# Kernel optimization log

Measured on AMD Instinct MI355X. Metric: run time of the kernel, lower is better.

The kernel has to match this reference:

```python
import jax, jax.numpy as jnp
import numpy as np

D_MODEL = 1024
NUM_HEADS = 16
THETA = 10000.0
NEG = -1000000.0  # masked_fill value used by the torch code


def _rope(x, token_positions, theta):
    # x: [B, H, S, d_head]; token_positions: [S] int
    d_k = x.shape[-1]
    half = d_k // 2
    j = jnp.arange(half, dtype=jnp.float32)
    inv_freq = theta ** (-(2.0 * j) / d_k)                      # [half]
    ang = token_positions.astype(jnp.float32)[:, None] * inv_freq  # [S, half]
    cos = jnp.cos(ang)
    sin = jnp.sin(ang)
    xp = x.reshape(x.shape[:-1] + (half, 2))  # adjacent pairs (pc, 2)
    x0, x1 = xp[..., 0], xp[..., 1]
    o0 = x0 * cos - x1 * sin
    o1 = x0 * sin + x1 * cos
    out = jnp.stack([o0, o1], axis=-1)
    return out.reshape(x.shape)


def setup_inputs() -> dict:
    key = jax.random.key(0)
    k0, k1, k2 = jax.random.split(key, 3)
    B, S, D = 2, 2048, D_MODEL
    std = (2.0 / (D + D)) ** 0.5
    X = jax.random.normal(k0, (B, S, D), dtype=jnp.float32)
    QKV_weights = jax.random.normal(k1, (3 * D, D), dtype=jnp.float32) * std
    O_weights = jax.random.normal(k2, (D, D), dtype=jnp.float32) * std
    token_positions = jnp.arange(S, dtype=jnp.int32)
    return {"X": X, "token_positions": token_positions,
            "QKV_weights": QKV_weights, "O_weights": O_weights}


def reference(X, token_positions, QKV_weights, O_weights):
    B, S, D = X.shape
    H = NUM_HEADS
    dh = D // H
    qkv = jnp.einsum('od,bsd->bso', QKV_weights, X)  # [B, S, 3D]
    Q, K, V = jnp.split(qkv, 3, axis=-1)

    def split_heads(t):
        return t.reshape(B, S, H, dh).transpose(0, 2, 1, 3)  # [B,H,S,dh]

    Q, K, V = split_heads(Q), split_heads(K), split_heads(V)
    Q = _rope(Q, token_positions, THETA)
    K = _rope(K, token_positions, THETA)

    scores = (jnp.einsum('bhqd,bhkd->bhqk', Q, K) / jnp.sqrt(jnp.float32(dh))).astype(jnp.float32)
    causal = jnp.tril(jnp.ones((S, S), dtype=bool))
    scores = jnp.where(causal, scores, NEG)
    probs = jax.nn.softmax(scores, axis=-1)
    attn = jnp.einsum('bhqk,bhkd->bhqd', probs, V.astype(jnp.float32)).astype(Q.dtype)
    attn = attn.transpose(0, 2, 1, 3).reshape(B, S, D)
    return jnp.einsum('od,bsd->bso', O_weights, attn)
```

## Files before the change

### kernel.cpp

```cpp
#include <hip/hip_runtime.h>
#include <math.h>

#define S_LEN 2048

using bf16x8  = __attribute__((ext_vector_type(8))) short;
using shortx4 = __attribute__((ext_vector_type(4))) short;
using f32x4   = __attribute__((ext_vector_type(4))) float;
using uintx4  = __attribute__((ext_vector_type(4))) unsigned;
using uintx2  = __attribute__((ext_vector_type(2))) unsigned;

static __device__ __forceinline__ short f2bf(float f) {
  unsigned u = __float_as_uint(f);
  u += 0x7fffu + ((u >> 16) & 1u);
  return (short)(u >> 16);
}

#if __has_builtin(__builtin_amdgcn_cvt_pk_bf16_f32)
using bf16x2_t = __attribute__((ext_vector_type(2))) __bf16;
static __device__ __forceinline__ unsigned pkbf(float a, float b) {
  bf16x2_t v = __builtin_amdgcn_cvt_pk_bf16_f32(a, b);
  return __builtin_bit_cast(unsigned, v);
}
#else
static __device__ __forceinline__ unsigned pkbf(float a, float b) {
  return (unsigned)(unsigned short)f2bf(a) | ((unsigned)(unsigned short)f2bf(b) << 16);
}
#endif

#define GLD_LDS16(gptr, lptr)                                                  \
  __builtin_amdgcn_global_load_lds(                                            \
      (__attribute__((address_space(1))) void*)(gptr),                         \
      (__attribute__((address_space(3))) void*)(lptr), 16, 0, 0)

#define EXP2_SHIFT 20.0f

static __device__ __forceinline__ f32x4 exp2s4(f32x4 a) {
  return (f32x4){__builtin_amdgcn_exp2f(a[0] - EXP2_SHIFT),
                 __builtin_amdgcn_exp2f(a[1] - EXP2_SHIFT),
                 __builtin_amdgcn_exp2f(a[2] - EXP2_SHIFT),
                 __builtin_amdgcn_exp2f(a[3] - EXP2_SHIFT)};
}

static __device__ __forceinline__ int sigma64(int k) {
  return (k & 0x20) | ((k & 0x0C) << 1) | ((k & 0x10) >> 2) | (k & 3);
}

__global__ __launch_bounds__(256) void init_kernel(const float* __restrict__ X,
                                                   const float* __restrict__ W1,
                                                   const float* __restrict__ W2,
                                                   const int* __restrict__ tok,
                                                   short* __restrict__ Xb,
                                                   short* __restrict__ W1b,
                                                   short* __restrict__ W2b,
                                                   float2* __restrict__ table) {
  if (blockIdx.x < 4096) {
    size_t idx = (size_t)(blockIdx.x * 256 + threadIdx.x) * 8;
    const float* src;
    short* dst;
    size_t off;
    if (idx < 4194304) { src = X; dst = Xb; off = idx; }
    else if (idx < 4194304 + 3145728) { src = W1; dst = W1b; off = idx - 4194304; }
    else { src = W2; dst = W2b; off = idx - (4194304 + 3145728); }
    float4 a = *(const float4*)(src + off);
    float4 b = *(const float4*)(src + off + 4);
    bf16x8 o = {f2bf(a.x), f2bf(a.y), f2bf(a.z), f2bf(a.w),
                f2bf(b.x), f2bf(b.y), f2bf(b.z), f2bf(b.w)};
    *(bf16x8*)(dst + off) = o;
  } else {
    int i = (blockIdx.x - 4096) * 256 + threadIdx.x;
    int s = i >> 5, j = i & 31;
    double pos = (double)tok[s];
    double ang = pos * pow(10000.0, -(double)j / 32.0);
    table[i] = make_float2((float)cos(ang), (float)sin(ang));
  }
}

template <int BM, typename OutT, int EPI>
__global__ __launch_bounds__(256) void gemm_ll(const short* __restrict__ A,
                                               const short* __restrict__ B,
                                               OutT* __restrict__ C,
                                               const float2* __restrict__ tab,
                                               short* __restrict__ Qb,
                                               short* __restrict__ Kb,
                                               short* __restrict__ VT,
                                               int M, int N, int K) {
  constexpr int MI = BM / 32;
  constexpr int AI = BM / 64;
  __shared__ short As[BM * 32];
  __shared__ short Bs[128 * 32];
  const int tid  = threadIdx.x;
  const int lane = tid & 63;
  const int wv   = tid >> 6;
  const int wm   = (wv >> 1) * (BM / 2);
  const int wn   = (wv & 1) * 64;
  const int m16  = lane & 15;
  const int q4   = lane >> 4;

  const int nwg = gridDim.x * gridDim.y;
  int bid = blockIdx.y * gridDim.x + blockIdx.x;
  bid = (bid & 7) * (nwg >> 3) + (bid >> 3);
  const int rowBase = (bid / gridDim.x) * BM;
  const int colBase = (bid % gridDim.x) * 128;

  const int lrow = lane >> 2;
  const int lchk = (lane & 3) ^ ((lane >> 3) & 3);
  const int fsw  = (q4 ^ ((m16 >> 1) & 3)) * 8;

  f32x4 acc[MI][4];
#pragma unroll
  for (int i = 0; i < MI; ++i)
#pragma unroll
    for (int j = 0; j < 4; ++j) acc[i][j] = (f32x4){0.f, 0.f, 0.f, 0.f};

  const short* Agl = A + (size_t)rowBase * K;
  const short* Bgl = B + (size_t)colBase * K;

  for (int kk = 0; kk < K; kk += 32) {
#pragma unroll
    for (int i = 0; i < AI; ++i) {
      const int r0 = (wv * AI + i) * 16;
      GLD_LDS16(Agl + (size_t)(r0 + lrow) * K + kk + lchk * 8, &As[r0 * 32]);
    }
#pragma unroll
    for (int i = 0; i < 2; ++i) {
      const int r0 = (wv * 2 + i) * 16;
      GLD_LDS16(Bgl + (size_t)(r0 + lrow) * K + kk + lchk * 8, &Bs[r0 * 32]);
    }
    __syncthreads();

    bf16x8 af[MI], bfv[4];
#pragma unroll
    for (int mi = 0; mi < MI; ++mi)
      af[mi] = *(const bf16x8*)&As[(wm + mi * 16 + m16) * 32 + fsw];
#pragma unroll
    for (int ni = 0; ni < 4; ++ni)
      bfv[ni] = *(const bf16x8*)&Bs[(wn + ni * 16 + m16) * 32 + fsw];
#pragma unroll
    for (int mi = 0; mi < MI; ++mi)
#pragma unroll
      for (int ni = 0; ni < 4; ++ni)
        acc[mi][ni] = __builtin_amdgcn_mfma_f32_16x16x32_bf16(af[mi], bfv[ni], acc[mi][ni], 0, 0, 0);
    __syncthreads();
  }

  if constexpr (EPI == 0) {
#pragma unroll
    for (int mi = 0; mi < MI; ++mi)
#pragma unroll
      for (int ni = 0; ni < 4; ++ni) {
        const int rbase = rowBase + wm + mi * 16 + q4 * 4;
        const int cidx  = colBase + wn + ni * 16 + m16;
#pragma unroll
        for (int r = 0; r < 4; ++r) {
          float v = acc[mi][ni][r];
          if constexpr (sizeof(OutT) == 2)
            C[(size_t)(rbase + r) * N + cidx] = (OutT)f2bf(v);
          else
            C[(size_t)(rbase + r) * N + cidx] = (OutT)v;
        }
      }
  } else {
    const int sect = colBase >> 10;
#pragma unroll
    for (int mi = 0; mi < MI; ++mi)
#pragma unroll
      for (int ni = 0; ni < 4; ++ni) {
        const int col = colBase + wn + ni * 16 + m16;
        const int rb  = rowBase + wm + mi * 16 + q4 * 4;
        if (sect == 2) {
          const int hd = col - 2048;
          const int h = hd >> 6, d = hd & 63;
          const int b = rb >> 11, s0 = rb & (S_LEN - 1);
          shortx4 pk4 = {f2bf(acc[mi][ni][0]), f2bf(acc[mi][ni][1]),
                         f2bf(acc[mi][ni][2]), f2bf(acc[mi][ni][3])};
          *(shortx4*)(VT + ((size_t)((b * 16 + h) * 64 + d)) * S_LEN +
                      (s0 & ~63) + sigma64(s0 & 63)) = pk4;
        } else {
          const int cc = col & 1023;
          const int h = cc >> 6, d = cc & 63, j = d >> 1;
          const float sgn = (m16 & 1) ? 1.f : -1.f;
          short* dstp = (sect == 0) ? Qb : Kb;
          const float scl = (sect == 0) ? (0.125f * 1.44269504f) : 1.f;
#pragma unroll
          for (int r = 0; r < 4; ++r) {
            const int row = rb + r;
            const int s = row & (S_LEN - 1), bidx = row >> 11;
            float2 cs = tab[s * 32 + j];
            float self = acc[mi][ni][r];
            float part = __shfl_xor(self, 1);
            float o = (self * cs.x + sgn * part * cs.y) * scl;
            dstp[((size_t)((bidx * 16 + h) * S_LEN + s)) * 64 + d] = f2bf(o);
          }
        }
      }
  }
}

__global__ __launch_bounds__(256, 2) void attn_mfma(const short* __restrict__ Qb,
                                                    const short* __restrict__ Kb,
                                                    const short* __restrict__ VT,
                                                    short* __restrict__ attnb) {
  __shared__ __align__(16) short Smem[9216];
  short* Ks = Smem;
  short* Vs = Smem + 64 * 72;
  const int tid  = threadIdx.x;
  const int lane = tid & 63;
  const int w    = tid >> 6;
  const int m16  = lane & 15;
  const int q4   = lane >> 4;
  const int bh   = blockIdx.x;
  const int jtx  = blockIdx.y;
  const int jt   = (jtx < 8) ? (15 - jtx) : (jtx - 8);
  const int b    = bh >> 4, h = bh & 15;
  const short* Qh = Qb + (size_t)bh * S_LEN * 64;
  const short* Kh = Kb + (size_t)bh * S_LEN * 64;
  const short* Vh = VT + (size_t)bh * 64 * S_LEN;

  const int srow = tid >> 3;
  const int seg  = tid & 7;

  const bf16x8 ones = {16256, 16256, 16256, 16256, 16256, 16256, 16256, 16256};

  const int q0 = jt * 128;
  const int ktiles = 2 * jt + 2;

  bf16x8 qf[2][2];
#pragma unroll
  for (int n = 0; n < 2; ++n)
#pragma unroll
    for (int ks = 0; ks < 2; ++ks)
      qf[n][ks] = *(const bf16x8*)(Qh + (size_t)(q0 + w * 32 + n * 16 + m16) * 64 + ks * 32 + q4 * 8);

  f32x4 O[2][4], Lacc[2];
#pragma unroll
  for (int n = 0; n < 2; ++n) {
    Lacc[n] = (f32x4){0.f, 0.f, 0.f, 0.f};
#pragma unroll
    for (int c = 0; c < 4; ++c) O[n][c] = (f32x4){0.f, 0.f, 0.f, 0.f};
  }

  bf16x8 kst[2], vst[2];
#pragma unroll
  for (int i = 0; i < 2; ++i) {
    kst[i] = *(const bf16x8*)(Kh + (size_t)(i * 32 + srow) * 64 + seg * 8);
    vst[i] = *(const bf16x8*)(Vh + (size_t)(i * 32 + srow) * S_LEN + seg * 8);
  }

  for (int t = 0; t < ktiles; ++t) {
#pragma unroll
    for (int i = 0; i < 2; ++i) {
      *(bf16x8*)&Ks[(i * 32 + srow) * 72 + seg * 8] = kst[i];
      *(bf16x8*)&Vs[(i * 32 + srow) * 72 + seg * 8] = vst[i];
    }
    __syncthreads();

    if (t + 1 < ktiles) {
#pragma unroll
      for (int i = 0; i < 2; ++i) {
        kst[i] = *(const bf16x8*)(Kh + (size_t)((t + 1) * 64 + i * 32 + srow) * 64 + seg * 8);
        vst[i] = *(const bf16x8*)(Vh + (size_t)(i * 32 + srow) * S_LEN + (t + 1) * 64 + seg * 8);
      }
    }

    f32x4 sc[2][4];
#pragma unroll
    for (int n = 0; n < 2; ++n)
#pragma unroll
      for (int c = 0; c < 4; ++c) sc[n][c] = (f32x4){0.f, 0.f, 0.f, 0.f};
    __builtin_amdgcn_s_setprio(1);
#pragma unroll
    for (int ks = 0; ks < 2; ++ks) {
#pragma unroll
      for (int c = 0; c < 4; ++c) {
        bf16x8 kf = *(const bf16x8*)&Ks[(c * 16 + m16) * 72 + ks * 32 + q4 * 8];
#pragma unroll
        for (int n = 0; n < 2; ++n)
          sc[n][c] = __builtin_amdgcn_mfma_f32_16x16x32_bf16(kf, qf[n][ks], sc[n][c], 0, 0, 0);
      }
    }
    __builtin_amdgcn_s_setprio(0);

    if (t >= ktiles - 2) {
#pragma unroll
      for (int n = 0; n < 2; ++n)
#pragma unroll
        for (int c = 0; c < 4; ++c) {
          const int qg = q0 + w * 32 + n * 16 + m16;
#pragma unroll
          for (int rr = 0; rr < 4; ++rr) {
            const int kg = t * 64 + c * 16 + q4 * 4 + rr;
            if (kg > qg) sc[n][c][rr] = -1e30f;
          }
        }
    }

    bf16x8 pb[2][2];
#pragma unroll
    for (int n = 0; n < 2; ++n) {
#pragma unroll
      for (int c = 0; c < 4; ++c) sc[n][c] = exp2s4(sc[n][c]);
      uintx4 u0 = {pkbf(sc[n][0][0], sc[n][0][1]), pkbf(sc[n][0][2], sc[n][0][3]),
                   pkbf(sc[n][1][0], sc[n][1][1]), pkbf(sc[n][1][2], sc[n][1][3])};
      uintx4 u1 = {pkbf(sc[n][2][0], sc[n][2][1]), pkbf(sc[n][2][2], sc[n][2][3]),
                   pkbf(sc[n][3][0], sc[n][3][1]), pkbf(sc[n][3][2], sc[n][3][3])};
      pb[n][0] = __builtin_bit_cast(bf16x8, u0);
      pb[n][1] = __builtin_bit_cast(bf16x8, u1);
    }

    __builtin_amdgcn_s_setprio(1);
#pragma unroll
    for (int ch = 0; ch < 2; ++ch) {
#pragma unroll
      for (int c2 = 0; c2 < 4; ++c2) {
        bf16x8 va = *(const bf16x8*)&Vs[(c2 * 16 + m16) * 72 + ch * 32 + q4 * 8];
#pragma unroll
        for (int n = 0; n < 2; ++n)
          O[n][c2] = __builtin_amdgcn_mfma_f32_16x16x32_bf16(va, pb[n][ch], O[n][c2], 0, 0, 0);
      }
#pragma unroll
      for (int n = 0; n < 2; ++n)
        Lacc[n] = __builtin_amdgcn_mfma_f32_16x16x32_bf16(ones, pb[n][ch], Lacc[n], 0, 0, 0);
    }
    __builtin_amdgcn_s_setprio(0);
    __syncthreads();
  }

#pragma unroll
  for (int n = 0; n < 2; ++n) {
    const float inv = __frcp_rn(Lacc[n][0]);
#pragma unroll
    for (int c2 = 0; c2 < 4; ++c2) {
      uintx2 uo = {pkbf(O[n][c2][0] * inv, O[n][c2][1] * inv),
                   pkbf(O[n][c2][2] * inv, O[n][c2][3] * inv)};
      *(shortx4*)&Smem[(w * 32 + n * 16 + m16) * 72 + c2 * 16 + q4 * 4] =
          __builtin_bit_cast(shortx4, uo);
    }
  }
  __syncthreads();
  {
    const int row = tid >> 1, hf = tid & 1;
    const short* src = &Smem[row * 72 + hf * 32];
    short* dst = attnb + (size_t)(b * S_LEN + q0 + row) * 1024 + h * 64 + hf * 32;
    ((bf16x8*)dst)[0] = ((const bf16x8*)src)[0];
    ((bf16x8*)dst)[1] = ((const bf16x8*)src)[1];
    ((bf16x8*)dst)[2] = ((const bf16x8*)src)[2];
    ((bf16x8*)dst)[3] = ((const bf16x8*)src)[3];
  }
}

extern "C" void kernel_launch(void* const* d_in, const int* in_sizes, int n_in,
                              void* d_out, int out_size, void* d_ws, size_t ws_size,
                              hipStream_t stream) {
  const float* X    = (const float*)d_in[0];
  const int*   tok  = (const int*)d_in[1];
  const float* Wqkv = (const float*)d_in[2];
  const float* Wo   = (const float*)d_in[3];
  float* out = (float*)d_out;

  char* w = (char*)d_ws;
  float2* table = (float2*)w;
  short*  Qb    = (short*)(w + 524288);
  short*  Kb    = Qb + 4194304;
  short*  VTt   = Kb + 4194304;
  short*  Xb    = VTt + 2 * 4194304;
  short*  Wqkvb = Xb + 4194304;
  short*  Wob   = Wqkvb + 3145728;
  short*  attnb = Wob + 1048576;

  hipLaunchKernelGGL(init_kernel, dim3(4352), dim3(256), 0, stream,
                     X, Wqkv, Wo, tok, Xb, Wqkvb, Wob, table);
  hipLaunchKernelGGL((gemm_ll<128, short, 1>), dim3(24, 32), dim3(256), 0, stream,
                     Xb, Wqkvb, (short*)nullptr, table, Qb, Kb, VTt, 4096, 3072, 1024);
  hipLaunchKernelGGL(attn_mfma, dim3(32, 16), dim3(256), 0, stream,
                     Qb, Kb, VTt, attnb);
  hipLaunchKernelGGL((gemm_ll<64, float, 0>), dim3(8, 64), dim3(256), 0, stream,
                     attnb, Wob, out, (const float2*)nullptr,
                     (short*)nullptr, (short*)nullptr, (short*)nullptr,
                     4096, 1024, 1024);
}
```

Baseline: 178.2 us.

## Double-buffer LDS in GEMM and attention to overlap loads with MFMA

The GEMM now uses two LDS buffers per operand. It issues the global-to-LDS loads for the next K slice before computing on the current one, with the loop unrolled by two, and it raises wave priority around the MFMA block. The attention kernel alternates between two K/V LDS buffers, which lets it drop the trailing per-tile barrier. This is meant to hide load latency and cut barrier stalls, at the cost of twice the LDS, which may lower occupancy.

Measured after the change: 174.0 us, median of 5. 2.4% less time.

```diff
diff --git a/kernel.cpp b/kernel.cpp
--- a/kernel.cpp
+++ b/kernel.cpp
@@ -86,8 +86,8 @@
                                                int M, int N, int K) {
   constexpr int MI = BM / 32;
   constexpr int AI = BM / 64;
-  __shared__ short As[BM * 32];
-  __shared__ short Bs[128 * 32];
+  __shared__ short As[2][BM * 32];
+  __shared__ short Bs[2][128 * 32];
   const int tid  = threadIdx.x;
   const int lane = tid & 63;
   const int wv   = tid >> 6;
@@ -112,36 +112,61 @@
 #pragma unroll
     for (int j = 0; j < 4; ++j) acc[i][j] = (f32x4){0.f, 0.f, 0.f, 0.f};
 
-  const short* Agl = A + (size_t)rowBase * K;
-  const short* Bgl = B + (size_t)colBase * K;
-
-  for (int kk = 0; kk < K; kk += 32) {
-#pragma unroll
-    for (int i = 0; i < AI; ++i) {
-      const int r0 = (wv * AI + i) * 16;
-      GLD_LDS16(Agl + (size_t)(r0 + lrow) * K + kk + lchk * 8, &As[r0 * 32]);
-    }
-#pragma unroll
-    for (int i = 0; i < 2; ++i) {
-      const int r0 = (wv * 2 + i) * 16;
-      GLD_LDS16(Bgl + (size_t)(r0 + lrow) * K + kk + lchk * 8, &Bs[r0 * 32]);
-    }
+  const short* ap[AI];
+  const short* bp[2];
+#pragma unroll
+  for (int i = 0; i < AI; ++i)
+    ap[i] = A + (size_t)(rowBase + (wv * AI + i) * 16 + lrow) * K + lchk * 8;
+#pragma unroll
+  for (int i = 0; i < 2; ++i)
+    bp[i] = B + (size_t)(colBase + (wv * 2 + i) * 16 + lrow) * K + lchk * 8;
+
+#define STAGE(buf)                                                             \
+  do {                                                                         \
+    _Pragma("unroll")                                                          \
+    for (int i = 0; i < AI; ++i) {                                             \
+      GLD_LDS16(ap[i], &As[buf][(wv * AI + i) * 512]);                         \
+      ap[i] += 32;                                                             \
+    }                                                                          \
+    _Pragma("unroll")                                                          \
+    for (int i = 0; i < 2; ++i) {                                              \
+      GLD_LDS16(bp[i], &Bs[buf][(wv * 2 + i) * 512]);                          \
+      bp[i] += 32;                                                             \
+    }                                                                          \
+  } while (0)
+
+#define COMPUTE(buf)                                                           \
+  do {                                                                         \
+    bf16x8 af[MI], bfv[4];                                                     \
+    _Pragma("unroll")                                                          \
+    for (int mi = 0; mi < MI; ++mi)                                            \
+      af[mi] = *(const bf16x8*)&As[buf][(wm + mi * 16 + m16) * 32 + fsw];      \
+    _Pragma("unroll")                                                          \
+    for (int ni = 0; ni < 4; ++ni)                                             \
+      bfv[ni] = *(const bf16x8*)&Bs[buf][(wn + ni * 16 + m16) * 32 + fsw];     \
+    __builtin_amdgcn_s_setprio(1);                                             \
+    _Pragma("unroll")                                                          \
+    for (int mi = 0; mi < MI; ++mi)                                            \
+      _Pragma("unroll")                                                        \
+      for (int ni = 0; ni < 4; ++ni)                                           \
+        acc[mi][ni] = __builtin_amdgcn_mfma_f32_16x16x32_bf16(                 \
+            af[mi], bfv[ni], acc[mi][ni], 0, 0, 0);                            \
+    __builtin_amdgcn_s_setprio(0);                                             \
+  } while (0)
+
+  STAGE(0);
+  __syncthreads();
+
+  for (int kk = 0; kk < K; kk += 64) {
+    STAGE(1);
+    COMPUTE(0);
     __syncthreads();
-
-    bf16x8 af[MI], bfv[4];
-#pragma unroll
-    for (int mi = 0; mi < MI; ++mi)
-      af[mi] = *(const bf16x8*)&As[(wm + mi * 16 + m16) * 32 + fsw];
-#pragma unroll
-    for (int ni = 0; ni < 4; ++ni)
-      bfv[ni] = *(const bf16x8*)&Bs[(wn + ni * 16 + m16) * 32 + fsw];
-#pragma unroll
-    for (int mi = 0; mi < MI; ++mi)
-#pragma unroll
-      for (int ni = 0; ni < 4; ++ni)
-        acc[mi][ni] = __builtin_amdgcn_mfma_f32_16x16x32_bf16(af[mi], bfv[ni], acc[mi][ni], 0, 0, 0);
+    if (kk + 64 < K) STAGE(0);
+    COMPUTE(1);
     __syncthreads();
   }
+#undef STAGE
+#undef COMPUTE
 
   if constexpr (EPI == 0) {
 #pragma unroll
@@ -200,9 +225,7 @@
                                                     const short* __restrict__ Kb,
                                                     const short* __restrict__ VT,
                                                     short* __restrict__ attnb) {
-  __shared__ __align__(16) short Smem[9216];
-  short* Ks = Smem;
-  short* Vs = Smem + 64 * 72;
+  __shared__ __align__(16) short Smem[18432];
   const int tid  = threadIdx.x;
   const int lane = tid & 63;
   const int w    = tid >> 6;
@@ -239,26 +262,36 @@
     for (int c = 0; c < 4; ++c) O[n][c] = (f32x4){0.f, 0.f, 0.f, 0.f};
   }
 
+  const short* kp[2];
+  const short* vp[2];
+#pragma unroll
+  for (int i = 0; i < 2; ++i) {
+    kp[i] = Kh + (size_t)(i * 32 + srow) * 64 + seg * 8;
+    vp[i] = Vh + (size_t)(i * 32 + srow) * S_LEN + seg * 8;
+  }
+
   bf16x8 kst[2], vst[2];
 #pragma unroll
   for (int i = 0; i < 2; ++i) {
-    kst[i] = *(const bf16x8*)(Kh + (size_t)(i * 32 + srow) * 64 + seg * 8);
-    vst[i] = *(const bf16x8*)(Vh + (size_t)(i * 32 + srow) * S_LEN + seg * 8);
+    kst[i] = *(const bf16x8*)kp[i];  kp[i] += 4096;
+    vst[i] = *(const bf16x8*)vp[i];  vp[i] += 64;
   }
 
   for (int t = 0; t < ktiles; ++t) {
+    short* Kc = Smem + (t & 1) * 9216;
+    short* Vc = Kc + 64 * 72;
 #pragma unroll
     for (int i = 0; i < 2; ++i) {
-      *(bf16x8*)&Ks[(i * 32 + srow) * 72 + seg * 8] = kst[i];
-      *(bf16x8*)&Vs[(i * 32 + srow) * 72 + seg * 8] = vst[i];
+      *(bf16x8*)&Kc[(i * 32 + srow) * 72 + seg * 8] = kst[i];
+      *(bf16x8*)&Vc[(i * 32 + srow) * 72 + seg * 8] = vst[i];
     }
     __syncthreads();
 
     if (t + 1 < ktiles) {
 #pragma unroll
       for (int i = 0; i < 2; ++i) {
-        kst[i] = *(const bf16x8*)(Kh + (size_t)((t + 1) * 64 + i * 32 + srow) * 64 + seg * 8);
-        vst[i] = *(const bf16x8*)(Vh + (size_t)(i * 32 + srow) * S_LEN + (t + 1) * 64 + seg * 8);
+        kst[i] = *(const bf16x8*)kp[i];  kp[i] += 4096;
+        vst[i] = *(const bf16x8*)vp[i];  vp[i] += 64;
       }
     }
 
@@ -272,7 +305,7 @@
     for (int ks = 0; ks < 2; ++ks) {
 #pragma unroll
       for (int c = 0; c < 4; ++c) {
-        bf16x8 kf = *(const bf16x8*)&Ks[(c * 16 + m16) * 72 + ks * 32 + q4 * 8];
+        bf16x8 kf = *(const bf16x8*)&Kc[(c * 16 + m16) * 72 + ks * 32 + q4 * 8];
 #pragma unroll
         for (int n = 0; n < 2; ++n)
           sc[n][c] = __builtin_amdgcn_mfma_f32_16x16x32_bf16(kf, qf[n][ks], sc[n][c], 0, 0, 0);
@@ -312,7 +345,7 @@
     for (int ch = 0; ch < 2; ++ch) {
 #pragma unroll
       for (int c2 = 0; c2 < 4; ++c2) {
-        bf16x8 va = *(const bf16x8*)&Vs[(c2 * 16 + m16) * 72 + ch * 32 + q4 * 8];
+        bf16x8 va = *(const bf16x8*)&Vc[(c2 * 16 + m16) * 72 + ch * 32 + q4 * 8];
 #pragma unroll
         for (int n = 0; n < 2; ++n)
           O[n][c2] = __builtin_amdgcn_mfma_f32_16x16x32_bf16(va, pb[n][ch], O[n][c2], 0, 0, 0);
@@ -322,7 +355,6 @@
         Lacc[n] = __builtin_amdgcn_mfma_f32_16x16x32_bf16(ones, pb[n][ch], Lacc[n], 0, 0, 0);
     }
     __builtin_amdgcn_s_setprio(0);
-    __syncthreads();
   }
 
 #pragma unroll
```
